# Optimization experiments

Measured on AMD Instinct MI355X. Metric: run time of the kernel, lower is better.

Reference implementation:

```python
import jax, jax.numpy as jnp
import numpy as np

C_CURV = 1.0      # manifold curvature c (= k in the torch code)
EPS = 1e-15
PROJ_EPS = 1e-5   # standard Poincare ball boundary eps for manifold.proj


def _clamp_abs(x, eps=EPS):
    return jnp.maximum(jnp.abs(x), eps) * jnp.sign(x)


def setup_inputs() -> dict:
    key = jax.random.key(0)
    k1, k2, k3 = jax.random.split(key, 3)
    B, D, C = 4096, 1024, 4096
    c = C_CURV
    x = jax.random.normal(k1, (B, D), dtype=jnp.float32)
    # reset_parameters(): a ~ N(0, D^-0.5 / sqrt(c)); p ~ N(0, 0.1) clipped to norm 0.9/sqrt(c)
    a = jax.random.normal(k2, (C, D), dtype=jnp.float32) * (D ** -0.5 / c ** 0.5)
    p = jax.random.normal(k3, (C, D), dtype=jnp.float32) * 0.1
    p_norm = jnp.linalg.norm(p, axis=1, keepdims=True)
    max_norm = 0.9 / jnp.sqrt(jnp.float32(c))
    p = p * jnp.minimum(max_norm / p_norm, 1.0)
    return {"x": x, "a": a, "p": p}


def _forward(x, a, p):
    k = jnp.float32(C_CURV)
    sqrt_k = jnp.sqrt(k)

    # manifold.proj: clip x to the open ball of radius (1 - eps)/sqrt(c)
    xn = jnp.maximum(jnp.linalg.norm(x, axis=-1, keepdims=True), EPS)
    maxn = (1.0 - PROJ_EPS) / sqrt_k
    x = jnp.where(xn > maxn, x * (maxn / xn), x)

    # Rank-structured Mobius addition: diff = mobius_add(-p, x) factors as
    #   diff[b,c,:] = (A[b,c] * (-p[c]) + Bc[c] * x[b]) / den[b,c]
    x2 = jnp.sum(x * x, axis=-1)          # [B]
    p2 = jnp.sum(p * p, axis=-1)          # [C]
    px = jnp.einsum('bd,cd->bc', x, p)    # [B,C]  <p_c, x_b>
    xa = jnp.einsum('bd,cd->bc', x, a)    # [B,C]  <a_c, x_b>
    pa = jnp.sum(p * a, axis=-1)          # [C]    <p_c, a_c>
    a_norm = jnp.sqrt(jnp.sum(a * a, axis=-1))  # [C]

    A = 1.0 - 2.0 * k * px + k * x2[:, None]                       # [B,C]
    Bc = 1.0 - k * p2                                              # [C]
    den = jnp.maximum(1.0 - 2.0 * k * px + (k * k) * x2[:, None] * p2[None, :], EPS)

    diff_norm2 = jnp.maximum(
        (A * A * p2[None, :] + (Bc * Bc)[None, :] * x2[:, None] - 2.0 * A * Bc[None, :] * px)
        / (den * den), EPS)                                        # [B,C]
    sc_diff_a = (-A * pa[None, :] + Bc[None, :] * xa) / den        # [B,C], signed

    num = 2.0 * sc_diff_a
    denom = _clamp_abs((1.0 + k * diff_norm2) * a_norm[None, :])
    distance = jnp.arcsinh(sqrt_k * num / denom) / sqrt_k
    return -distance  # logits [B,C]


def reference(x, a, p):
    return _forward(x, a, p)
```

## Files before the change

### kernel.cpp

```cpp
#include <hip/hip_runtime.h>
#include <hip/hip_bf16.h>
#include <math.h>


#define EPSF 1e-15f
#define MAXN 0.99999f

constexpr int Bdim = 4096;
constexpr int Ddim = 1024;
constexpr int Cdim = 4096;

typedef __bf16 bf16x8 __attribute__((ext_vector_type(8)));
typedef float  f32x4  __attribute__((ext_vector_type(4)));
typedef unsigned short u16;

__device__ __forceinline__ u16 f2bf(float f) {
  __hip_bfloat16 h = __float2bfloat16(f);
  return *reinterpret_cast<const u16*>(&h);
}

__device__ __forceinline__ void gl_lds16(const u16* g, u16* l) {
  __builtin_amdgcn_global_load_lds(
      (const __attribute__((address_space(1))) void*)g,
      (__attribute__((address_space(3))) void*)l, 16, 0, 0);
}


__global__ __launch_bounds__(256) void prep_x(const float* __restrict__ x,
                                              u16* __restrict__ xb,
                                              float* __restrict__ x2o) {
  const int b = blockIdx.x, t = threadIdx.x;
  float4 v = ((const float4*)(x + (size_t)b * Ddim))[t];
  float s = v.x * v.x + v.y * v.y + v.z * v.z + v.w * v.w;
  __shared__ float red[4];
#pragma unroll
  for (int o = 32; o > 0; o >>= 1) s += __shfl_down(s, o);
  if ((t & 63) == 0) red[t >> 6] = s;
  __syncthreads();
  s = red[0] + red[1] + red[2] + red[3];
  float norm  = sqrtf(s);
  float xn    = fmaxf(norm, EPSF);
  float scale = (xn > MAXN) ? (MAXN / xn) : 1.0f;
  if (t == 0) x2o[b] = s * scale * scale;
  ushort4 o4;
  o4.x = f2bf(v.x * scale); o4.y = f2bf(v.y * scale);
  o4.z = f2bf(v.z * scale); o4.w = f2bf(v.w * scale);
  ((ushort4*)(xb + (size_t)b * Ddim))[t] = o4;
}

__global__ __launch_bounds__(256) void prep_pa(const float* __restrict__ a,
                                               const float* __restrict__ p,
                                               u16* __restrict__ pab,
                                               float* __restrict__ p2o,
                                               float* __restrict__ pao,
                                               float* __restrict__ anio) {
  const int c = blockIdx.x, t = threadIdx.x;
  float4 av = ((const float4*)(a + (size_t)c * Ddim))[t];
  float4 pv = ((const float4*)(p + (size_t)c * Ddim))[t];
  float sp2 = pv.x * pv.x + pv.y * pv.y + pv.z * pv.z + pv.w * pv.w;
  float spa = pv.x * av.x + pv.y * av.y + pv.z * av.z + pv.w * av.w;
  float sa2 = av.x * av.x + av.y * av.y + av.z * av.z + av.w * av.w;
  __shared__ float red[12];
#pragma unroll
  for (int o = 32; o > 0; o >>= 1) {
    sp2 += __shfl_down(sp2, o);
    spa += __shfl_down(spa, o);
    sa2 += __shfl_down(sa2, o);
  }
  if ((t & 63) == 0) { int w = t >> 6; red[w] = sp2; red[4 + w] = spa; red[8 + w] = sa2; }
  __syncthreads();
  if (t == 0) {
    p2o[c]  = red[0] + red[1] + red[2] + red[3];
    pao[c]  = red[4] + red[5] + red[6] + red[7];
    anio[c] = 1.0f / sqrtf(red[8] + red[9] + red[10] + red[11]);
  }
  const int prP = ((c >> 4) << 5) + (c & 15);
  ushort4 oa, op;
  oa.x = f2bf(av.x); oa.y = f2bf(av.y); oa.z = f2bf(av.z); oa.w = f2bf(av.w);
  op.x = f2bf(pv.x); op.y = f2bf(pv.y); op.z = f2bf(pv.z); op.w = f2bf(pv.w);
  ((ushort4*)(pab + (size_t)prP * Ddim))[t]        = op;
  ((ushort4*)(pab + (size_t)(prP + 16) * Ddim))[t] = oa;
}


__global__ __launch_bounds__(256, 2) void gemm_ep(
    const u16* __restrict__ xb, const u16* __restrict__ pab,
    const float* __restrict__ x2g, const float* __restrict__ p2g,
    const float* __restrict__ pag, const float* __restrict__ anig,
    float* __restrict__ out) {
  __shared__ u16 Xs[3][8192];
  __shared__ u16 PAs[3][4096];

  const int t = threadIdx.x;

  const int flat  = blockIdx.y * 64 + blockIdx.x;
  const int swz   = (flat & 7) * 128 + (flat >> 3);
  const int chunk = swz >> 7;
  const int local = swz & 127;
  const int by = chunk * 2 + (local >> 6);
  const int bx = local & 63;

  const int lane = t & 63;
  const int wid  = t >> 6;
  const int wr   = wid >> 1;
  const int wc   = wid & 1;

  const int r0  = t >> 2;
  const int sw8 = ((t & 3) ^ ((r0 >> 1) & 3)) * 8;
  const u16* xsrc  = xb  + (size_t)(by * 256 + r0) * Ddim + sw8;
  const u16* pasrc = pab + (size_t)(bx * 128 + r0) * Ddim + sw8;
  const int t8 = t * 8;
  const size_t q64 = (size_t)64 * Ddim;

  const int arow = wr * 128 + (lane & 15);
  const int brow = wc * 64  + (lane & 15);
  const int aoff = arow * 32 + (((lane >> 4) ^ ((arow >> 1) & 3)) * 8);
  const int boff = brow * 32 + (((lane >> 4) ^ ((brow >> 1) & 3)) * 8);

  f32x4 acc[8][4];
  const f32x4 zero = {0.f, 0.f, 0.f, 0.f};
#pragma unroll
  for (int m = 0; m < 8; ++m)
#pragma unroll
    for (int n = 0; n < 4; ++n) acc[m][n] = zero;

#define STAGE(SLOT) do {                                              \
    u16* Xw  = (u16*)&Xs[(SLOT)][0];                                  \
    u16* PAw = (u16*)&PAs[(SLOT)][0];                                 \
    gl_lds16(xgp,            Xw + t8);                                \
    gl_lds16(xgp + q64,      Xw + 2048 + t8);                         \
    gl_lds16(xgp + 2 * q64,  Xw + 4096 + t8);                         \
    gl_lds16(xgp + 3 * q64,  Xw + 6144 + t8);                         \
    gl_lds16(pgp,            PAw + t8);                               \
    gl_lds16(pgp + q64,      PAw + 2048 + t8);                        \
    xgp += 32; pgp += 32;                                             \
  } while (0)

#define COMPUTE(SLOT) do {                                            \
    const u16* Xr  = &Xs[(SLOT)][0];                                  \
    const u16* PAr = &PAs[(SLOT)][0];                                 \
    bf16x8 bv0 = *(const bf16x8*)&PAr[boff];                          \
    bf16x8 bv1 = *(const bf16x8*)&PAr[boff + 512];                    \
    bf16x8 bv2 = *(const bf16x8*)&PAr[boff + 1024];                   \
    bf16x8 bv3 = *(const bf16x8*)&PAr[boff + 1536];                   \
    bf16x8 a0 = *(const bf16x8*)&Xr[aoff];                            \
    bf16x8 a1 = *(const bf16x8*)&Xr[aoff + 512];                      \
    bf16x8 a2 = *(const bf16x8*)&Xr[aoff + 1024];                     \
    bf16x8 a3 = *(const bf16x8*)&Xr[aoff + 1536];                     \
    bf16x8 a4 = *(const bf16x8*)&Xr[aoff + 2048];                     \
    bf16x8 a5 = *(const bf16x8*)&Xr[aoff + 2560];                     \
    bf16x8 a6 = *(const bf16x8*)&Xr[aoff + 3072];                     \
    bf16x8 a7 = *(const bf16x8*)&Xr[aoff + 3584];                     \
    __builtin_amdgcn_s_setprio(1);                                    \
    _Pragma("unroll")                                                 \
    for (int n = 0; n < 4; ++n) {                                     \
      bf16x8 bv = (n == 0) ? bv0 : (n == 1) ? bv1 : (n == 2) ? bv2 : bv3; \
      acc[0][n] = __builtin_amdgcn_mfma_f32_16x16x32_bf16(a0, bv, acc[0][n], 0, 0, 0); \
      acc[1][n] = __builtin_amdgcn_mfma_f32_16x16x32_bf16(a1, bv, acc[1][n], 0, 0, 0); \
      acc[2][n] = __builtin_amdgcn_mfma_f32_16x16x32_bf16(a2, bv, acc[2][n], 0, 0, 0); \
      acc[3][n] = __builtin_amdgcn_mfma_f32_16x16x32_bf16(a3, bv, acc[3][n], 0, 0, 0); \
      acc[4][n] = __builtin_amdgcn_mfma_f32_16x16x32_bf16(a4, bv, acc[4][n], 0, 0, 0); \
      acc[5][n] = __builtin_amdgcn_mfma_f32_16x16x32_bf16(a5, bv, acc[5][n], 0, 0, 0); \
      acc[6][n] = __builtin_amdgcn_mfma_f32_16x16x32_bf16(a6, bv, acc[6][n], 0, 0, 0); \
      acc[7][n] = __builtin_amdgcn_mfma_f32_16x16x32_bf16(a7, bv, acc[7][n], 0, 0, 0); \
    }                                                                 \
    __builtin_amdgcn_s_setprio(0);                                    \
  } while (0)

#define GATE_BAR(N) do {                                              \
    asm volatile("s_waitcnt vmcnt(" #N ")" ::: "memory");             \
    __builtin_amdgcn_s_barrier();                                     \
    __builtin_amdgcn_sched_barrier(0);                                \
  } while (0)

  const u16* xgp = xsrc;
  const u16* pgp = pasrc;
  STAGE(0);
  STAGE(1);

  for (int g = 0; g < 10; ++g) {
    GATE_BAR(6);  STAGE(2);  COMPUTE(0);
    GATE_BAR(6);  STAGE(0);  COMPUTE(1);
    GATE_BAR(6);  STAGE(1);  COMPUTE(2);
  }
  GATE_BAR(6);  COMPUTE(0);
  GATE_BAR(0);  COMPUTE(1);

#undef GATE_BAR
#undef STAGE
#undef COMPUTE

#pragma unroll
  for (int m = 0; m < 8; ++m) {
    const int rl0 = by * 256 + wr * 128 + m * 16 + (lane >> 4) * 4;
    const float4 x2r4 = *(const float4*)&x2g[rl0];
    float x2r[4] = {x2r4.x, x2r4.y, x2r4.z, x2r4.w};
#pragma unroll
    for (int g = 0; g < 2; ++g) {
      const int cl = bx * 64 + wc * 32 + g * 16 + (lane & 15);
      const float p2c = p2g[cl];
      const float pac = pag[cl];
      const float ani = anig[cl];
      const float Bcc = 1.0f - p2c;
      f32x4 px4 = acc[m][2 * g];
      f32x4 xa4 = acc[m][2 * g + 1];
#pragma unroll
      for (int j = 0; j < 4; ++j) {
        const float px = px4[j];
        const float xa = xa4[j];
        const float Av   = 1.0f - 2.0f * px + x2r[j];
        const float den  = fmaxf(1.0f - 2.0f * px + x2r[j] * p2c, EPSF);
        const float rden = __builtin_amdgcn_rcpf(den);
        const float dn2  = fmaxf((Av * Av * p2c + Bcc * Bcc * x2r[j] - 2.0f * Av * Bcc * px) * rden * rden, EPSF);
        const float sc   = (Bcc * xa - Av * pac) * rden;
        const float z    = 2.0f * sc * ani * __builtin_amdgcn_rcpf(1.0f + dn2);
        const float z2 = z * z;
        float r;
        if (z2 > 0.04f) r = asinhf(z);
        else            r = z * (1.0f - z2 * (1.0f / 6.0f) + z2 * z2 * 0.075f);
        out[(size_t)rl0 * Cdim + j * Cdim + cl] = -r;
      }
    }
  }
}

extern "C" void kernel_launch(void* const* d_in, const int* in_sizes, int n_in,
                              void* d_out, int out_size, void* d_ws, size_t ws_size,
                              hipStream_t stream) {
  const float* x = (const float*)d_in[0];
  const float* a = (const float*)d_in[1];
  const float* p = (const float*)d_in[2];
  float* out = (float*)d_out;

  char* ws = (char*)d_ws;
  u16* xb  = (u16*)(ws);
  u16* pab = (u16*)(ws + (size_t)8 * 1024 * 1024);
  float* x2  = (float*)(ws + (size_t)24 * 1024 * 1024);
  float* p2  = x2 + Bdim;
  float* pa  = p2 + Cdim;
  float* ani = pa + Cdim;

  prep_x <<<Bdim, 256, 0, stream>>>(x, xb, x2);
  prep_pa<<<Cdim, 256, 0, stream>>>(a, p, pab, p2, pa, ani);
  gemm_ep<<<dim3(64, 16), 256, 0, stream>>>(xb, pab, x2, p2, pa, ani, out);
}
```

Baseline: 110.9 us.

## Replace LDS-staged GEMM pipeline with direct global-to-register fragment loads

Removes the shared-memory triple buffer, the global_load_lds staging and the barriers. Each wave now loads its MFMA fragments straight from global memory into registers, double-buffered in two register sets. The block-index swizzle is also changed to a different tile traversal order. This drops LDS traffic and synchronization but makes each wave fetch data that is shared across waves without reuse, and the 16-byte per-lane row-strided loads are poorly coalesced. It also raises register pressure.

```diff
diff --git a/kernel.cpp b/kernel.cpp
--- a/kernel.cpp
+++ b/kernel.cpp
@@ -17,12 +17,6 @@
 __device__ __forceinline__ u16 f2bf(float f) {
   __hip_bfloat16 h = __float2bfloat16(f);
   return *reinterpret_cast<const u16*>(&h);
-}
-
-__device__ __forceinline__ void gl_lds16(const u16* g, u16* l) {
-  __builtin_amdgcn_global_load_lds(
-      (const __attribute__((address_space(1))) void*)g,
-      (__attribute__((address_space(3))) void*)l, 16, 0, 0);
 }
 
 
@@ -88,34 +82,22 @@
     const float* __restrict__ x2g, const float* __restrict__ p2g,
     const float* __restrict__ pag, const float* __restrict__ anig,
     float* __restrict__ out) {
-  __shared__ u16 Xs[3][8192];
-  __shared__ u16 PAs[3][4096];
-
   const int t = threadIdx.x;
 
   const int flat  = blockIdx.y * 64 + blockIdx.x;
   const int swz   = (flat & 7) * 128 + (flat >> 3);
   const int chunk = swz >> 7;
   const int local = swz & 127;
-  const int by = chunk * 2 + (local >> 6);
-  const int bx = local & 63;
+  const int bx = chunk * 8 + (local & 7);
+  const int by = local >> 3;
 
   const int lane = t & 63;
   const int wid  = t >> 6;
   const int wr   = wid >> 1;
   const int wc   = wid & 1;
 
-  const int r0  = t >> 2;
-  const int sw8 = ((t & 3) ^ ((r0 >> 1) & 3)) * 8;
-  const u16* xsrc  = xb  + (size_t)(by * 256 + r0) * Ddim + sw8;
-  const u16* pasrc = pab + (size_t)(bx * 128 + r0) * Ddim + sw8;
-  const int t8 = t * 8;
-  const size_t q64 = (size_t)64 * Ddim;
-
-  const int arow = wr * 128 + (lane & 15);
-  const int brow = wc * 64  + (lane & 15);
-  const int aoff = arow * 32 + (((lane >> 4) ^ ((arow >> 1) & 3)) * 8);
-  const int boff = brow * 32 + (((lane >> 4) ^ ((brow >> 1) & 3)) * 8);
+  const u16* xA = xb  + (size_t)(by * 256 + wr * 128 + (lane & 15)) * Ddim + (lane >> 4) * 8;
+  const u16* pB = pab + (size_t)(bx * 128 + wc * 64  + (lane & 15)) * Ddim + (lane >> 4) * 8;
 
   f32x4 acc[8][4];
   const f32x4 zero = {0.f, 0.f, 0.f, 0.f};
@@ -124,71 +106,60 @@
 #pragma unroll
     for (int n = 0; n < 4; ++n) acc[m][n] = zero;
 
-#define STAGE(SLOT) do {                                              \
-    u16* Xw  = (u16*)&Xs[(SLOT)][0];                                  \
-    u16* PAw = (u16*)&PAs[(SLOT)][0];                                 \
-    gl_lds16(xgp,            Xw + t8);                                \
-    gl_lds16(xgp + q64,      Xw + 2048 + t8);                         \
-    gl_lds16(xgp + 2 * q64,  Xw + 4096 + t8);                         \
-    gl_lds16(xgp + 3 * q64,  Xw + 6144 + t8);                         \
-    gl_lds16(pgp,            PAw + t8);                               \
-    gl_lds16(pgp + q64,      PAw + 2048 + t8);                        \
-    xgp += 32; pgp += 32;                                             \
+  struct F {
+    bf16x8 a0, a1, a2, a3, a4, a5, a6, a7;
+    bf16x8 b0, b1, b2, b3;
+  };
+  F fA, fB;
+
+#define RS (16 * 1024)
+
+#define LOADF(FS, KO) do {                                            \
+    FS.a0 = *(const bf16x8*)(xA + 0 * RS + (KO));                     \
+    FS.a1 = *(const bf16x8*)(xA + 1 * RS + (KO));                     \
+    FS.a2 = *(const bf16x8*)(xA + 2 * RS + (KO));                     \
+    FS.a3 = *(const bf16x8*)(xA + 3 * RS + (KO));                     \
+    FS.a4 = *(const bf16x8*)(xA + 4 * RS + (KO));                     \
+    FS.a5 = *(const bf16x8*)(xA + 5 * RS + (KO));                     \
+    FS.a6 = *(const bf16x8*)(xA + 6 * RS + (KO));                     \
+    FS.a7 = *(const bf16x8*)(xA + 7 * RS + (KO));                     \
+    FS.b0 = *(const bf16x8*)(pB + 0 * RS + (KO));                     \
+    FS.b1 = *(const bf16x8*)(pB + 1 * RS + (KO));                     \
+    FS.b2 = *(const bf16x8*)(pB + 2 * RS + (KO));                     \
+    FS.b3 = *(const bf16x8*)(pB + 3 * RS + (KO));                     \
   } while (0)
 
-#define COMPUTE(SLOT) do {                                            \
-    const u16* Xr  = &Xs[(SLOT)][0];                                  \
-    const u16* PAr = &PAs[(SLOT)][0];                                 \
-    bf16x8 bv0 = *(const bf16x8*)&PAr[boff];                          \
-    bf16x8 bv1 = *(const bf16x8*)&PAr[boff + 512];                    \
-    bf16x8 bv2 = *(const bf16x8*)&PAr[boff + 1024];                   \
-    bf16x8 bv3 = *(const bf16x8*)&PAr[boff + 1536];                   \
-    bf16x8 a0 = *(const bf16x8*)&Xr[aoff];                            \
-    bf16x8 a1 = *(const bf16x8*)&Xr[aoff + 512];                      \
-    bf16x8 a2 = *(const bf16x8*)&Xr[aoff + 1024];                     \
-    bf16x8 a3 = *(const bf16x8*)&Xr[aoff + 1536];                     \
-    bf16x8 a4 = *(const bf16x8*)&Xr[aoff + 2048];                     \
-    bf16x8 a5 = *(const bf16x8*)&Xr[aoff + 2560];                     \
-    bf16x8 a6 = *(const bf16x8*)&Xr[aoff + 3072];                     \
-    bf16x8 a7 = *(const bf16x8*)&Xr[aoff + 3584];                     \
+#define MFMA32(FS) do {                                               \
     __builtin_amdgcn_s_setprio(1);                                    \
     _Pragma("unroll")                                                 \
     for (int n = 0; n < 4; ++n) {                                     \
-      bf16x8 bv = (n == 0) ? bv0 : (n == 1) ? bv1 : (n == 2) ? bv2 : bv3; \
-      acc[0][n] = __builtin_amdgcn_mfma_f32_16x16x32_bf16(a0, bv, acc[0][n], 0, 0, 0); \
-      acc[1][n] = __builtin_amdgcn_mfma_f32_16x16x32_bf16(a1, bv, acc[1][n], 0, 0, 0); \
-      acc[2][n] = __builtin_amdgcn_mfma_f32_16x16x32_bf16(a2, bv, acc[2][n], 0, 0, 0); \
-      acc[3][n] = __builtin_amdgcn_mfma_f32_16x16x32_bf16(a3, bv, acc[3][n], 0, 0, 0); \
-      acc[4][n] = __builtin_amdgcn_mfma_f32_16x16x32_bf16(a4, bv, acc[4][n], 0, 0, 0); \
-      acc[5][n] = __builtin_amdgcn_mfma_f32_16x16x32_bf16(a5, bv, acc[5][n], 0, 0, 0); \
-      acc[6][n] = __builtin_amdgcn_mfma_f32_16x16x32_bf16(a6, bv, acc[6][n], 0, 0, 0); \
-      acc[7][n] = __builtin_amdgcn_mfma_f32_16x16x32_bf16(a7, bv, acc[7][n], 0, 0, 0); \
+      bf16x8 bv = (n == 0) ? FS.b0 : (n == 1) ? FS.b1 : (n == 2) ? FS.b2 : FS.b3; \
+      acc[0][n] = __builtin_amdgcn_mfma_f32_16x16x32_bf16(FS.a0, bv, acc[0][n], 0, 0, 0); \
+      acc[1][n] = __builtin_amdgcn_mfma_f32_16x16x32_bf16(FS.a1, bv, acc[1][n], 0, 0, 0); \
+      acc[2][n] = __builtin_amdgcn_mfma_f32_16x16x32_bf16(FS.a2, bv, acc[2][n], 0, 0, 0); \
+      acc[3][n] = __builtin_amdgcn_mfma_f32_16x16x32_bf16(FS.a3, bv, acc[3][n], 0, 0, 0); \
+      acc[4][n] = __builtin_amdgcn_mfma_f32_16x16x32_bf16(FS.a4, bv, acc[4][n], 0, 0, 0); \
+      acc[5][n] = __builtin_amdgcn_mfma_f32_16x16x32_bf16(FS.a5, bv, acc[5][n], 0, 0, 0); \
+      acc[6][n] = __builtin_amdgcn_mfma_f32_16x16x32_bf16(FS.a6, bv, acc[6][n], 0, 0, 0); \
+      acc[7][n] = __builtin_amdgcn_mfma_f32_16x16x32_bf16(FS.a7, bv, acc[7][n], 0, 0, 0); \
     }                                                                 \
     __builtin_amdgcn_s_setprio(0);                                    \
   } while (0)
 
-#define GATE_BAR(N) do {                                              \
-    asm volatile("s_waitcnt vmcnt(" #N ")" ::: "memory");             \
-    __builtin_amdgcn_s_barrier();                                     \
-    __builtin_amdgcn_sched_barrier(0);                                \
-  } while (0)
-
-  const u16* xgp = xsrc;
-  const u16* pgp = pasrc;
-  STAGE(0);
-  STAGE(1);
-
-  for (int g = 0; g < 10; ++g) {
-    GATE_BAR(6);  STAGE(2);  COMPUTE(0);
-    GATE_BAR(6);  STAGE(0);  COMPUTE(1);
-    GATE_BAR(6);  STAGE(1);  COMPUTE(2);
-  }
-  GATE_BAR(6);  COMPUTE(0);
-  GATE_BAR(0);  COMPUTE(1);
-
-#undef GATE_BAR
-#undef STAGE
-#undef COMPUTE
+  LOADF(fA, 0);
+  for (int kt = 0; kt < 30; kt += 2) {
+    LOADF(fB, (kt + 1) * 32);
+    MFMA32(fA);
+    LOADF(fA, (kt + 2) * 32);
+    MFMA32(fB);
+  }
+  LOADF(fB, 31 * 32);
+  MFMA32(fA);
+  MFMA32(fB);
+
+#undef LOADF
+#undef MFMA32
+#undef RS
 
 #pragma unroll
   for (int m = 0; m < 8; ++m) {
```

Result: slower. 208.5 us (+88.0%).
